# Performance work log

Hardware: AMD Instinct MI355X
Metric: run time of the kernel (lower is better)

The kernel has to match this reference:

```python
import jax, jax.numpy as jnp
import numpy as np

SHAPE0 = (256, 256)   # top pyramid level (h, w)
SIGMA = 3.0
EPS = 1e-3
BATCH = 128
N_CHAN = 3
N_LEVELS = 4
N_PIX = sum((SHAPE0[0] >> i) * (SHAPE0[1] >> i) for i in range(N_LEVELS))  # 87040


def _gauss_lum_kernel(sigma):
    # 2D Gaussian times RGB luminance weights -> HWIO kernel (kh, kw, 3, 1)
    s = int(np.ceil(2 * sigma))
    u = np.linspace(-s, s, 2 * s + 1)
    g = np.exp(-(u[:, None] ** 2 + u[None, :] ** 2) / (2 * sigma ** 2)) / (2 * np.pi * sigma ** 2)
    w = np.array([0.2989, 0.587, 0.114])
    k = (g[:, :, None, None] * w[None, None, :, None]).astype(np.float32)
    return jnp.asarray(k)


def _conv_same(x, k):
    # NHWC conv with zero 'SAME' padding; equivalent to the original
    # pad(s) + SAME conv + center crop (net effect is SAME with zero pad).
    return jax.lax.conv_general_dilated(
        x, k, window_strides=(1, 1), padding='SAME',
        dimension_numbers=('NHWC', 'HWIO', 'NHWC'))


def setup_inputs() -> dict:
    key = jax.random.key(0)
    x = jax.random.uniform(key, (BATCH, N_PIX, N_CHAN), dtype=jnp.float32)
    return {"x": x}


def reference(x):
    k = _gauss_lum_kernel(SIGMA)
    n_pix, nc = x.shape[1], x.shape[2]
    h, w = SHAPE0
    outs = []
    i = 0
    while i + h * w <= n_pix:  # static Python loop over pyramid levels
        xi = x[:, i:i + h * w, :].reshape(-1, h, w, nc)          # (B,h,w,3)
        lum = _conv_same(xi, k)                                   # (B,h,w,1)
        dens = _conv_same(jnp.ones((1, h, w, nc), x.dtype), k)    # (1,h,w,1), input-independent
        outs.append((xi / (lum / dens + EPS)).reshape(-1, h * w, nc))
        i += h * w
        h //= 2
        w //= 2
    return jnp.concatenate(outs, axis=1)  # packed pyramid (B, n_pix, 3)
```

## Files before the change

kernel.cpp:

```cpp
#include <hip/hip_runtime.h>


#define NPIX   87040
#define EPSV   1e-3f
#define WSUM   0.9999f
#define TW     64
#define TH     32
#define RAD    6
#define RW     (TW + 2*RAD)
#define RH     (TH + 2*RAD)

__device__ __constant__ float G1[13] = {
    0.01799699f, 0.03315904f, 0.05467002f, 0.08065689f, 0.10648267f,
    0.12579441f, 0.13298076f, 0.12579441f, 0.10648267f, 0.08065689f,
    0.05467002f, 0.03315904f, 0.01799699f
};
__device__ __constant__ float PRE[14] = {
    0.00000000f, 0.01799699f, 0.05115603f, 0.10582605f, 0.18648294f,
    0.29296561f, 0.41876002f, 0.55174078f, 0.67753519f, 0.78401786f,
    0.86467475f, 0.91934477f, 0.95250381f, 0.97050080f
};

__global__ __launch_bounds__(256)
void mslln_kernel(const float* __restrict__ x, float* __restrict__ out) {
    __shared__ float s_lum[RH][RW];
    __shared__ float s_rc[RH][TW];

    const int bid = blockIdx.x;
    const int t   = threadIdx.x;

    int img, tl, txlog, h, off;
    if (bid < 4096)      { img = bid >> 5;          tl = bid & 31;         txlog = 2; h = 256; off = 0;     }
    else if (bid < 5120) { int r = bid - 4096; img = r >> 3; tl = r & 7;   txlog = 1; h = 128; off = 65536; }
    else if (bid < 5376) { int r = bid - 5120; img = r >> 1; tl = r & 1;   txlog = 0; h = 64;  off = 81920; }
    else                 { img = bid - 5376;        tl = 0;                txlog = 0; h = 32;  off = 86016; }
    const int w   = h;
    const int tx0 = (tl & ((1 << txlog) - 1)) << 6;
    const int ty0 = (tl >> txlog) << 5;

    const float* __restrict__ xb = x   + (size_t)img * (NPIX * 3) + (size_t)off * 3;
    float*       __restrict__ ob = out + (size_t)img * (NPIX * 3) + (size_t)off * 3;

    float rr[8], rg[8], rb[8];
#pragma unroll
    for (int k = 0; k < 8; k++) {
        int p  = t + k * 256;
        int lx = p & 63, ly = p >> 6;
        int gy = ty0 + ly, gx = tx0 + lx;
        float r = 0.f, g = 0.f, b = 0.f;
        if (gx < w) {
            int idx = (gy * w + gx) * 3;
            r = xb[idx]; g = xb[idx + 1]; b = xb[idx + 2];
        }
        rr[k] = r; rg[k] = g; rb[k] = b;
        s_lum[ly + RAD][lx + RAD] = 0.2989f * r + 0.587f * g + 0.114f * b;
    }

    for (int i = t; i < RH * RW; i += 256) {
        int ry = i / RW;
        int rx = i - ry * RW;
        if (ry >= RAD && ry < RAD + TH && rx >= RAD && rx < RAD + TW) continue;
        int gy = ty0 + ry - RAD, gx = tx0 + rx - RAD;
        float lum = 0.f;
        if (gy >= 0 && gy < h && gx >= 0 && gx < w) {
            int idx = (gy * w + gx) * 3;
            lum = 0.2989f * xb[idx] + 0.587f * xb[idx + 1] + 0.114f * xb[idx + 2];
        }
        s_lum[ry][rx] = lum;
    }
    __syncthreads();

    for (int i = t; i < RH * TW; i += 256) {
        int r0 = i >> 6, c = i & 63;
        float sum = 0.f;
#pragma unroll
        for (int j = 0; j < 13; j++) sum += s_lum[r0][c + j] * G1[j];
        s_rc[r0][c] = sum;
    }
    __syncthreads();

#pragma unroll
    for (int k = 0; k < 8; k++) {
        int p  = t + k * 256;
        int lx = p & 63, ly = p >> 6;
        int gy = ty0 + ly, gx = tx0 + lx;
        if (gx >= w) continue;
        float lum = 0.f;
#pragma unroll
        for (int j = 0; j < 13; j++) lum += s_rc[ly + j][lx] * G1[j];
        int ylo = min(RAD, gy), yhi = min(RAD, h - 1 - gy);
        int xlo = min(RAD, gx), xhi = min(RAD, w - 1 - gx);
        float Sy = PRE[RAD + yhi + 1] - PRE[RAD - ylo];
        float Sx = PRE[RAD + xhi + 1] - PRE[RAD - xlo];
        float dens  = WSUM * Sy * Sx;
        float scale = 1.0f / (lum / dens + EPSV);
        int idx = (gy * w + gx) * 3;
        ob[idx]     = rr[k] * scale;
        ob[idx + 1] = rg[k] * scale;
        ob[idx + 2] = rb[k] * scale;
    }
}

extern "C" void kernel_launch(void* const* d_in, const int* in_sizes, int n_in,
                              void* d_out, int out_size, void* d_ws, size_t ws_size,
                              hipStream_t stream) {
    const float* x = (const float*)d_in[0];
    float* out = (float*)d_out;
    mslln_kernel<<<5504, 256, 0, stream>>>(x, out);
}
```

Baseline: 272.7 us.

## Halve tile height, vectorize RGB loads with float4, stage scale in LDS

Tile height drops from 32 to 16 rows, which doubles the block count. Input loads change from scalar per-pixel RGB reads to float4 groups of 4 pixels, and the halo region is padded to an 80-wide, 4-aligned buffer so loads stay vectorized. The per-pixel scale is written to shared memory, and the final pass reloads x as float4 from global memory to write vectorized outputs. This targets uncoalesced scalar stride-3 accesses, but it adds a second global read of x and a larger relative halo overhead from the smaller tiles.

After: 244.9 us. 1.11x faster.

```diff
diff --git a/kernel.cpp b/kernel.cpp
--- a/kernel.cpp
+++ b/kernel.cpp
@@ -5,10 +5,11 @@
 #define EPSV   1e-3f
 #define WSUM   0.9999f
 #define TW     64
-#define TH     32
+#define TH     16
 #define RAD    6
-#define RW     (TW + 2*RAD)
-#define RH     (TH + 2*RAD)
+#define LW     80
+#define LH     28
+#define NG     (LH * 20)
 
 __device__ __constant__ float G1[13] = {
     0.01799699f, 0.03315904f, 0.05467002f, 0.08065689f, 0.10648267f,
@@ -23,81 +24,109 @@
 
 __global__ __launch_bounds__(256)
 void mslln_kernel(const float* __restrict__ x, float* __restrict__ out) {
-    __shared__ float s_lum[RH][RW];
-    __shared__ float s_rc[RH][TW];
+    __shared__ float s_lum[LH][LW];
+    __shared__ float s_rc[LH][TW];
+    __shared__ float s_scale[TH][TW];
 
     const int bid = blockIdx.x;
     const int t   = threadIdx.x;
 
     int img, tl, txlog, h, off;
-    if (bid < 4096)      { img = bid >> 5;          tl = bid & 31;         txlog = 2; h = 256; off = 0;     }
-    else if (bid < 5120) { int r = bid - 4096; img = r >> 3; tl = r & 7;   txlog = 1; h = 128; off = 65536; }
-    else if (bid < 5376) { int r = bid - 5120; img = r >> 1; tl = r & 1;   txlog = 0; h = 64;  off = 81920; }
-    else                 { img = bid - 5376;        tl = 0;                txlog = 0; h = 32;  off = 86016; }
+    if (bid < 8192)       { img = bid >> 6;                 tl = bid & 63; txlog = 2; h = 256; off = 0;     }
+    else if (bid < 10240) { int r = bid - 8192;  img = r >> 4; tl = r & 15; txlog = 1; h = 128; off = 65536; }
+    else if (bid < 10752) { int r = bid - 10240; img = r >> 2; tl = r & 3;  txlog = 0; h = 64;  off = 81920; }
+    else                  { int r = bid - 10752; img = r >> 1; tl = r & 1;  txlog = 0; h = 32;  off = 86016; }
     const int w   = h;
     const int tx0 = (tl & ((1 << txlog) - 1)) << 6;
-    const int ty0 = (tl >> txlog) << 5;
+    const int ty0 = (tl >> txlog) << 4;
 
     const float* __restrict__ xb = x   + (size_t)img * (NPIX * 3) + (size_t)off * 3;
     float*       __restrict__ ob = out + (size_t)img * (NPIX * 3) + (size_t)off * 3;
 
-    float rr[8], rg[8], rb[8];
 #pragma unroll
-    for (int k = 0; k < 8; k++) {
-        int p  = t + k * 256;
-        int lx = p & 63, ly = p >> 6;
-        int gy = ty0 + ly, gx = tx0 + lx;
-        float r = 0.f, g = 0.f, b = 0.f;
-        if (gx < w) {
-            int idx = (gy * w + gx) * 3;
-            r = xb[idx]; g = xb[idx + 1]; b = xb[idx + 2];
+    for (int k = 0; k < 3; k++) {
+        unsigned i = t + k * 256;
+        if (i < NG) {
+            int gr  = i / 20;
+            int gc  = i - gr * 20;
+            int gy  = ty0 + gr - RAD;
+            int gx0 = tx0 + (gc << 2) - 8;
+            float4 f0 = {0,0,0,0}, f1 = {0,0,0,0}, f2 = {0,0,0,0};
+            if (gy >= 0 && gy < h) {
+                if (gx0 >= 0 && gx0 + 3 < w) {
+                    const float4* p = (const float4*)(xb + ((size_t)gy * w + gx0) * 3);
+                    f0 = p[0]; f1 = p[1]; f2 = p[2];
+                } else {
+                    float v[12];
+#pragma unroll
+                    for (int c = 0; c < 12; c++) v[c] = 0.f;
+#pragma unroll
+                    for (int c = 0; c < 4; c++) {
+                        int gx = gx0 + c;
+                        if (gx >= 0 && gx < w) {
+                            const float* s = xb + ((size_t)gy * w + gx) * 3;
+                            v[3*c] = s[0]; v[3*c+1] = s[1]; v[3*c+2] = s[2];
+                        }
+                    }
+                    f0 = make_float4(v[0], v[1], v[2],  v[3]);
+                    f1 = make_float4(v[4], v[5], v[6],  v[7]);
+                    f2 = make_float4(v[8], v[9], v[10], v[11]);
+                }
+            }
+            float l0 = 0.2989f*f0.x + 0.587f*f0.y + 0.114f*f0.z;
+            float l1 = 0.2989f*f0.w + 0.587f*f1.x + 0.114f*f1.y;
+            float l2 = 0.2989f*f1.z + 0.587f*f1.w + 0.114f*f2.x;
+            float l3 = 0.2989f*f2.y + 0.587f*f2.z + 0.114f*f2.w;
+            *(float4*)&s_lum[gr][gc << 2] = make_float4(l0, l1, l2, l3);
         }
-        rr[k] = r; rg[k] = g; rb[k] = b;
-        s_lum[ly + RAD][lx + RAD] = 0.2989f * r + 0.587f * g + 0.114f * b;
-    }
-
-    for (int i = t; i < RH * RW; i += 256) {
-        int ry = i / RW;
-        int rx = i - ry * RW;
-        if (ry >= RAD && ry < RAD + TH && rx >= RAD && rx < RAD + TW) continue;
-        int gy = ty0 + ry - RAD, gx = tx0 + rx - RAD;
-        float lum = 0.f;
-        if (gy >= 0 && gy < h && gx >= 0 && gx < w) {
-            int idx = (gy * w + gx) * 3;
-            lum = 0.2989f * xb[idx] + 0.587f * xb[idx + 1] + 0.114f * xb[idx + 2];
-        }
-        s_lum[ry][rx] = lum;
-    }
-    __syncthreads();
-
-    for (int i = t; i < RH * TW; i += 256) {
-        int r0 = i >> 6, c = i & 63;
-        float sum = 0.f;
-#pragma unroll
-        for (int j = 0; j < 13; j++) sum += s_lum[r0][c + j] * G1[j];
-        s_rc[r0][c] = sum;
     }
     __syncthreads();
 
 #pragma unroll
-    for (int k = 0; k < 8; k++) {
-        int p  = t + k * 256;
-        int lx = p & 63, ly = p >> 6;
-        int gy = ty0 + ly, gx = tx0 + lx;
-        if (gx >= w) continue;
-        float lum = 0.f;
+    for (int k = 0; k < 7; k++) {
+        int i = t + k * 256;
+        int r = i >> 6, c = i & 63;
+        float s = 0.f;
 #pragma unroll
-        for (int j = 0; j < 13; j++) lum += s_rc[ly + j][lx] * G1[j];
-        int ylo = min(RAD, gy), yhi = min(RAD, h - 1 - gy);
-        int xlo = min(RAD, gx), xhi = min(RAD, w - 1 - gx);
-        float Sy = PRE[RAD + yhi + 1] - PRE[RAD - ylo];
-        float Sx = PRE[RAD + xhi + 1] - PRE[RAD - xlo];
-        float dens  = WSUM * Sy * Sx;
-        float scale = 1.0f / (lum / dens + EPSV);
-        int idx = (gy * w + gx) * 3;
-        ob[idx]     = rr[k] * scale;
-        ob[idx + 1] = rg[k] * scale;
-        ob[idx + 2] = rb[k] * scale;
+        for (int j = 0; j < 13; j++) s += s_lum[r][c + 2 + j] * G1[j];
+        s_rc[r][c] = s;
+    }
+    __syncthreads();
+
+#pragma unroll
+    for (int k = 0; k < 4; k++) {
+        int i  = t + k * 256;
+        int ly = i >> 6, lx = i & 63;
+        if (tx0 + lx < w) {
+            float s = 0.f;
+#pragma unroll
+            for (int j = 0; j < 13; j++) s += s_rc[ly + j][lx] * G1[j];
+            int gy = ty0 + ly, gx = tx0 + lx;
+            int ylo = min(RAD, gy), yhi = min(RAD, h - 1 - gy);
+            int xlo = min(RAD, gx), xhi = min(RAD, w - 1 - gx);
+            float Sy = PRE[RAD + yhi + 1] - PRE[RAD - ylo];
+            float Sx = PRE[RAD + xhi + 1] - PRE[RAD - xlo];
+            float dens = WSUM * Sy * Sx;
+            s_scale[ly][lx] = 1.0f / (s / dens + EPSV);
+        }
+    }
+    __syncthreads();
+
+    {
+        int gr  = t >> 4;
+        int gc  = t & 15;
+        int gx0 = tx0 + (gc << 2);
+        if (gx0 < w) {
+            int gy = ty0 + gr;
+            const float4* p = (const float4*)(xb + ((size_t)gy * w + gx0) * 3);
+            float4 f0 = p[0], f1 = p[1], f2 = p[2];
+            float4 sc = *(const float4*)&s_scale[gr][gc << 2];
+            f0.x *= sc.x; f0.y *= sc.x; f0.z *= sc.x; f0.w *= sc.y;
+            f1.x *= sc.y; f1.y *= sc.y; f1.z *= sc.z; f1.w *= sc.z;
+            f2.x *= sc.z; f2.y *= sc.w; f2.z *= sc.w; f2.w *= sc.w;
+            float4* q = (float4*)(ob + ((size_t)gy * w + gx0) * 3);
+            q[0] = f0; q[1] = f1; q[2] = f2;
+        }
     }
 }
 
@@ -106,5 +135,5 @@
                               hipStream_t stream) {
     const float* x = (const float*)d_in[0];
     float* out = (float*)d_out;
-    mslln_kernel<<<5504, 256, 0, stream>>>(x, out);
+    mslln_kernel<<<11008, 256, 0, stream>>>(x, out);
 }
```
